# Optimization experiments

Measured on AMD Instinct MI355X. Metric: run time of the kernel, lower is better.

The kernel has to match this reference:

```python
import jax, jax.numpy as jnp
import numpy as np

B, N, H, NH = 2, 2048, 1024, 16
D = H // NH  # head_dim = 64


def setup_inputs() -> dict:
    key = jax.random.key(0)
    ks = jax.random.split(key, 12)
    s = 0.02
    inp = {
        'q': jax.random.normal(ks[0], (B, N, H), jnp.float32),
        'k': jax.random.normal(ks[1], (B, N, H), jnp.float32),
        'v': jax.random.normal(ks[2], (B, N, H), jnp.float32),
        # causal mask: 1 where attending allowed, 0 above diagonal
        'mask': jnp.tril(jnp.ones((N, N), jnp.float32))[None, None],
        'Wq': jax.random.normal(ks[3], (H, H), jnp.float32) * s,
        'bq': jnp.zeros((H,), jnp.float32),
        'Wk': jax.random.normal(ks[4], (H, H), jnp.float32) * s,
        'bk': jnp.zeros((H,), jnp.float32),
        'Wv': jax.random.normal(ks[5], (H, H), jnp.float32) * s,
        'bv': jnp.zeros((H,), jnp.float32),
        'Wp': jax.random.normal(ks[6], (H, H), jnp.float32) * s,
        'bp': jnp.zeros((H,), jnp.float32),
    }
    return inp


def _split_heads(x):
    # [b, n, (h d)] -> [b, h, n, d]
    b, n, _ = x.shape
    return x.reshape(b, n, NH, D).transpose(0, 2, 1, 3)


def reference(q, k, v, mask, Wq, bq, Wk, bk, Wv, bv, Wp, bp):
    # torch nn.Linear: x @ W.T + b
    Q = _split_heads(q @ Wq.T + bq)                      # [b, h, n, d]
    K = _split_heads(k @ Wk.T + bk)
    V = _split_heads(v @ Wv.T + bv)
    scores = jnp.einsum('bhnd,bhmd->bhnm', Q, K) / jnp.sqrt(jnp.float32(D))
    scores = jnp.where(mask == 0, -jnp.inf, scores)      # masked_fill
    attn = jax.nn.softmax(scores, axis=-1)
    out = jnp.einsum('bhnm,bhmd->bhnd', attn, V)         # [b, h, n, d]
    out = out.transpose(0, 2, 1, 3).reshape(q.shape[0], q.shape[1], H)
    # dropout is identity in eval mode
    return out @ Wp.T + bp
```

## Files before the change

kernel.cpp:

```cpp
#include <hip/hip_runtime.h>

typedef unsigned short u16;
typedef __attribute__((ext_vector_type(8))) short bf16x8;
typedef __attribute__((ext_vector_type(4))) short bf16x4;
typedef __attribute__((ext_vector_type(4))) float f32x4;

#define NB 2
#define SEQ 2048
#define HID 1024
#define NHEAD 16
#define HD 64
#define MROWS (NB * SEQ)

__device__ __forceinline__ u16 f2bf(float f) {
  union { float f; unsigned u; } x; x.f = f;
  unsigned r = x.u + 0x7fffu + ((x.u >> 16) & 1u);
  return (u16)(r >> 16);
}
__device__ __forceinline__ u16 f2bf_trunc(float f) {
  union { float f; unsigned u; } x; x.f = f;
  return (u16)(x.u >> 16);
}

#define GLOAD_LDS16(g, l)                                                   \
  __builtin_amdgcn_global_load_lds(                                         \
      (const __attribute__((address_space(1))) void*)(g),                   \
      (__attribute__((address_space(3))) void*)(l), 16, 0, 0)

__global__ __launch_bounds__(256)
void conv_all(const float* __restrict__ q, const float* __restrict__ k,
              const float* __restrict__ v, const float* __restrict__ wq,
              const float* __restrict__ wk, const float* __restrict__ wv,
              const float* __restrict__ wp, u16* __restrict__ qb,
              u16* __restrict__ kb, u16* __restrict__ vb,
              u16* __restrict__ wcat, u16* __restrict__ wpb)
{
  const int i = blockIdx.x * 256 + threadIdx.x;
  const float* s; u16* d;
  if (i < 1572864) {
    const int seg = i / 524288;
    const int off = i - seg * 524288;
    s = (seg == 0 ? q : seg == 1 ? k : v) + (size_t)off * 8;
    d = (seg == 0 ? qb : seg == 1 ? kb : vb) + (size_t)off * 8;
  } else {
    const int j = i - 1572864;
    const int seg = j / 131072;
    const int off = j - seg * 131072;
    s = (seg == 0 ? wq : seg == 1 ? wk : seg == 2 ? wv : wp) + (size_t)off * 8;
    d = (seg < 3 ? wcat + (size_t)seg * 1048576 : wpb) + (size_t)off * 8;
  }
  f32x4 a = *(const f32x4*)s;
  f32x4 b = *(const f32x4*)(s + 4);
  bf16x8 o;
#pragma unroll
  for (int j = 0; j < 4; ++j) { o[j] = (short)f2bf(a[j]); o[4 + j] = (short)f2bf(b[j]); }
  *(bf16x8*)d = o;
}

__global__ __launch_bounds__(256)
void gemm_qkv(const u16* __restrict__ A0, const u16* __restrict__ A1,
              const u16* __restrict__ A2, const u16* __restrict__ Wcat,
              const float* __restrict__ b0, const float* __restrict__ b1,
              const float* __restrict__ b2,
              u16* __restrict__ Qh, u16* __restrict__ Kh, u16* __restrict__ Vt,
              float qscale)
{
  __shared__ u16 As[2 * 128 * 64];
  __shared__ u16 Bs[2 * 128 * 64];
  const int p = blockIdx.x;
  const int c = p & 7;
  const int i_ = p >> 3;
  const int G = c * 12 + (i_ % 12);
  const int j = i_ / 12;
  const int g = G >> 5;
  const int m0 = (G & 31) * 128;
  const int n0 = (g * 8 + j) * 128;
  const u16* A = (g == 0) ? A0 : (g == 1) ? A1 : A2;
  const float* bias = (g == 0) ? b0 : (g == 1) ? b1 : b2;
  const int t = threadIdx.x, lane = t & 63, w = t >> 6;
  const int grp = lane >> 4, lr = lane & 15;
  const int wr = (w >> 1) * 64, wc = (w & 1) * 64;
  const int sw8 = lr & 7;

  f32x4 acc[4][4];
#pragma unroll
  for (int i = 0; i < 4; ++i)
#pragma unroll
    for (int j2 = 0; j2 < 4; ++j2) acc[i][j2] = (f32x4){0.f, 0.f, 0.f, 0.f};

  const int srow8 = lane >> 3;
  const int achunk = ((lane & 7) ^ srow8) * 8;
  const u16* ag = A + (size_t)(m0 + w * 32 + srow8) * HID + achunk;
  const u16* wg = Wcat + (size_t)(n0 + w * 32 + srow8) * HID + achunk;

#define STAGE(BI, K0)                                                \
  {                                                                  \
    const u16* ab = ag + (K0);                                       \
    const u16* wb = wg + (K0);                                       \
    u16* al = As + (BI) * 8192 + (w * 32) * 64;                      \
    u16* bl = Bs + (BI) * 8192 + (w * 32) * 64;                      \
    GLOAD_LDS16(ab, al);                                             \
    GLOAD_LDS16(ab + (size_t)8 * HID, al + 8 * 64);                  \
    GLOAD_LDS16(ab + (size_t)16 * HID, al + 16 * 64);                \
    GLOAD_LDS16(ab + (size_t)24 * HID, al + 24 * 64);                \
    GLOAD_LDS16(wb, bl);                                             \
    GLOAD_LDS16(wb + (size_t)8 * HID, bl + 8 * 64);                  \
    GLOAD_LDS16(wb + (size_t)16 * HID, bl + 16 * 64);                \
    GLOAD_LDS16(wb + (size_t)24 * HID, bl + 24 * 64);                \
  }

  STAGE(0, 0);

  for (int it = 0; it < 16; ++it) {
    const int cur = it & 1;
    asm volatile("s_waitcnt vmcnt(0)" ::: "memory");
    __builtin_amdgcn_s_barrier();
    __builtin_amdgcn_sched_barrier(0);
    asm volatile("" ::: "memory");
    if (it < 15) STAGE(cur ^ 1, (it + 1) * 64);
    const u16* Ab = As + cur * 8192;
    const u16* Bb = Bs + cur * 8192;
#pragma unroll
    for (int kh = 0; kh < 2; ++kh) {
      bf16x8 af[4], bf[4];
#pragma unroll
      for (int mi = 0; mi < 4; ++mi)
        af[mi] = *(const bf16x8*)&Ab[(wr + mi * 16 + lr) * 64 +
                                     (((kh * 4 + grp) ^ sw8) * 8)];
#pragma unroll
      for (int ni = 0; ni < 4; ++ni)
        bf[ni] = *(const bf16x8*)&Bb[(wc + ni * 16 + lr) * 64 +
                                     (((kh * 4 + grp) ^ sw8) * 8)];
      __builtin_amdgcn_s_setprio(1);
#pragma unroll
      for (int mi = 0; mi < 4; ++mi)
#pragma unroll
        for (int ni = 0; ni < 4; ++ni)
          acc[mi][ni] = __builtin_amdgcn_mfma_f32_16x16x32_bf16(
              af[mi], bf[ni], acc[mi][ni], 0, 0, 0);
      __builtin_amdgcn_s_setprio(0);
    }
  }
#undef STAGE

  const float scale = (g == 0) ? qscale : 1.f;
#pragma unroll
  for (int mi = 0; mi < 4; ++mi) {
#pragma unroll
    for (int ni = 0; ni < 4; ++ni) {
      const int nl = (n0 & (HID - 1)) + wc + ni * 16 + lr;
      const float bval = bias[nl];
      const int mb = m0 + wr + mi * 16 + grp * 4;
      const int h = nl >> 6, d = nl & (HD - 1);
      if (g == 2) {
        const int b = mb >> 11, nn = mb & (SEQ - 1);
        bf16x4 pk;
#pragma unroll
        for (int r = 0; r < 4; ++r)
          pk[r] = (short)f2bf(acc[mi][ni][r] + bval);
        *(bf16x4*)&Vt[((size_t)(b * NHEAD + h) * HD + d) * SEQ + nn] = pk;
      } else {
        u16* O = (g == 0) ? Qh : Kh;
#pragma unroll
        for (int r = 0; r < 4; ++r) {
          const int m = mb + r;
          const int b = m >> 11, nn = m & (SEQ - 1);
          O[((size_t)(b * NHEAD + h) * SEQ + nn) * HD + d] =
              f2bf((acc[mi][ni][r] + bval) * scale);
        }
      }
    }
  }
}

__global__ __launch_bounds__(256)
void gemm_proj(const u16* __restrict__ A, const u16* __restrict__ W,
               const float* __restrict__ bias, float* __restrict__ Op)
{
  __shared__ u16 As[2 * 128 * 64];
  __shared__ u16 Bs[2 * 128 * 64];
  const int p = blockIdx.x;
  const int c = p & 7;
  const int i_ = p >> 3;
  const int G = c * 4 + (i_ & 3);
  const int j = i_ >> 2;
  const int m0 = G * 128, n0 = j * 128;
  const int t = threadIdx.x, lane = t & 63, w = t >> 6;
  const int grp = lane >> 4, lr = lane & 15;
  const int wr = (w >> 1) * 64, wc = (w & 1) * 64;
  const int sw8 = lr & 7;

  f32x4 acc[4][4];
#pragma unroll
  for (int i = 0; i < 4; ++i)
#pragma unroll
    for (int j2 = 0; j2 < 4; ++j2) acc[i][j2] = (f32x4){0.f, 0.f, 0.f, 0.f};

  const int srow8 = lane >> 3;
  const int achunk = ((lane & 7) ^ srow8) * 8;
  const u16* ag = A + (size_t)(m0 + w * 32 + srow8) * HID + achunk;
  const u16* wg = W + (size_t)(n0 + w * 32 + srow8) * HID + achunk;

#define STAGE(BI, K0)                                                \
  {                                                                  \
    const u16* ab = ag + (K0);                                       \
    const u16* wb = wg + (K0);                                       \
    u16* al = As + (BI) * 8192 + (w * 32) * 64;                      \
    u16* bl = Bs + (BI) * 8192 + (w * 32) * 64;                      \
    GLOAD_LDS16(ab, al);                                             \
    GLOAD_LDS16(ab + (size_t)8 * HID, al + 8 * 64);                  \
    GLOAD_LDS16(ab + (size_t)16 * HID, al + 16 * 64);                \
    GLOAD_LDS16(ab + (size_t)24 * HID, al + 24 * 64);                \
    GLOAD_LDS16(wb, bl);                                             \
    GLOAD_LDS16(wb + (size_t)8 * HID, bl + 8 * 64);                  \
    GLOAD_LDS16(wb + (size_t)16 * HID, bl + 16 * 64);                \
    GLOAD_LDS16(wb + (size_t)24 * HID, bl + 24 * 64);                \
  }

  STAGE(0, 0);

  for (int it = 0; it < 16; ++it) {
    const int cur = it & 1;
    asm volatile("s_waitcnt vmcnt(0)" ::: "memory");
    __builtin_amdgcn_s_barrier();
    __builtin_amdgcn_sched_barrier(0);
    asm volatile("" ::: "memory");
    if (it < 15) STAGE(cur ^ 1, (it + 1) * 64);
    const u16* Ab = As + cur * 8192;
    const u16* Bb = Bs + cur * 8192;
#pragma unroll
    for (int kh = 0; kh < 2; ++kh) {
      bf16x8 af[4], bf[4];
#pragma unroll
      for (int mi = 0; mi < 4; ++mi)
        af[mi] = *(const bf16x8*)&Ab[(wr + mi * 16 + lr) * 64 +
                                     (((kh * 4 + grp) ^ sw8) * 8)];
#pragma unroll
      for (int ni = 0; ni < 4; ++ni)
        bf[ni] = *(const bf16x8*)&Bb[(wc + ni * 16 + lr) * 64 +
                                     (((kh * 4 + grp) ^ sw8) * 8)];
      __builtin_amdgcn_s_setprio(1);
#pragma unroll
      for (int mi = 0; mi < 4; ++mi)
#pragma unroll
        for (int ni = 0; ni < 4; ++ni)
          acc[mi][ni] = __builtin_amdgcn_mfma_f32_16x16x32_bf16(
              af[mi], bf[ni], acc[mi][ni], 0, 0, 0);
      __builtin_amdgcn_s_setprio(0);
    }
  }
#undef STAGE

#pragma unroll
  for (int mi = 0; mi < 4; ++mi) {
#pragma unroll
    for (int ni = 0; ni < 4; ++ni) {
      const int n = n0 + wc + ni * 16 + lr;
      const float bval = bias[n];
      const int mb = m0 + wr + mi * 16 + grp * 4;
#pragma unroll
      for (int r = 0; r < 4; ++r)
        Op[(size_t)(mb + r) * HID + n] = acc[mi][ni][r] + bval;
    }
  }
}

__global__ __launch_bounds__(512)
void attn_fwd(const u16* __restrict__ Q, const u16* __restrict__ K,
              const u16* __restrict__ Vt, u16* __restrict__ O)
{
  __shared__ u16 KB[2][4096];
  __shared__ u16 VB[2][4096];
  const int bh = blockIdx.y;
  const int t = threadIdx.x;
  const int w = t >> 6, lane = t & 63;
  const int grp = lane >> 4, lr = lane & 15;
  const int qtA = blockIdx.x;
  const int qtB = 15 - qtA;
  const int q0A = qtA * 128 + w * 16;
  const int q0B = qtB * 128 + w * 16;
  const int ntB = 2 * qtB + 2;
  const size_t base = (size_t)bh * SEQ * HD;
  const float NEGINF = -__builtin_inff();

  const int srow = lane >> 3;
  const int scol = (lane & 7) ^ srow;
  const u16* kg = K + base + (size_t)(w * 8 + srow) * HD + scol * 8;
  const u16* vg = Vt + base + (size_t)(w * 8 + srow) * SEQ + scol * 8;

  const bf16x8 aqA0 = *(const bf16x8*)&Q[base + (size_t)(q0A + lr) * HD + grp * 8];
  const bf16x8 aqA1 = *(const bf16x8*)&Q[base + (size_t)(q0A + lr) * HD + grp * 8 + 32];
  const bf16x8 aqB0 = *(const bf16x8*)&Q[base + (size_t)(q0B + lr) * HD + grp * 8];
  const bf16x8 aqB1 = *(const bf16x8*)&Q[base + (size_t)(q0B + lr) * HD + grp * 8 + 32];

  float lA = 0.f, lB = 0.f;
  f32x4 oA[4], oB[4];
#pragma unroll
  for (int c = 0; c < 4; ++c) {
    oA[c] = (f32x4){0.f, 0.f, 0.f, 0.f};
    oB[c] = (f32x4){0.f, 0.f, 0.f, 0.f};
  }

  const int idqA = q0A >> 6;
  const int idqB = q0B >> 6;
  const int sw = lr & 7;

#define STAGE(bi, j0)                                              \
  {                                                                \
    GLOAD_LDS16(kg + (size_t)(j0) * HD, &KB[bi][w * 512]);         \
    GLOAD_LDS16(vg + (j0), &VB[bi][w * 512]);                      \
  }

#define COMPUTE(Q0, AQ0, AQ1, OACC, LI, IDQ)                                  \
  do {                                                                        \
    f32x4 sv[4];                                                              \
    __builtin_amdgcn_s_setprio(1);                                            \
    _Pragma("unroll")                                                         \
    for (int st = 0; st < 4; ++st) {                                          \
      const int ro = (st * 16 + lr) * 64;                                     \
      bf16x8 k0 = *(const bf16x8*)&KB[bi][ro + ((grp ^ sw) * 8)];             \
      bf16x8 k1 = *(const bf16x8*)&KB[bi][ro + (((grp + 4) ^ sw) * 8)];       \
      f32x4 s = (f32x4){0.f, 0.f, 0.f, 0.f};                                  \
      s = __builtin_amdgcn_mfma_f32_16x16x32_bf16(k0, (AQ0), s, 0, 0, 0);     \
      s = __builtin_amdgcn_mfma_f32_16x16x32_bf16(k1, (AQ1), s, 0, 0, 0);     \
      sv[st] = s;                                                             \
    }                                                                         \
    __builtin_amdgcn_s_setprio(0);                                            \
    bf16x4 bv[4][4];                                                          \
    _Pragma("unroll")                                                         \
    for (int st = 0; st < 4; ++st)                                            \
      _Pragma("unroll")                                                       \
      for (int c = 0; c < 4; ++c)                                             \
        bv[st][c] = *(const bf16x4*)&VB[bi][(c * 16 + lr) * 64 +              \
                        (((st * 2 + (grp >> 1)) ^ sw) * 8) + (grp & 1) * 4];  \
    if (it == (IDQ)) {                                                        \
      const int j0 = it << 6, qg = (Q0) + lr;                                 \
      _Pragma("unroll")                                                       \
      for (int st = 0; st < 4; ++st)                                          \
        _Pragma("unroll")                                                     \
        for (int r = 0; r < 4; ++r)                                           \
          if (j0 + st * 16 + grp * 4 + r > qg) sv[st][r] = NEGINF;            \
    }                                                                         \
    float rs = 0.f;                                                           \
    _Pragma("unroll")                                                         \
    for (int st = 0; st < 4; ++st)                                            \
      _Pragma("unroll")                                                       \
      for (int r = 0; r < 4; ++r) {                                           \
        sv[st][r] = exp2f(sv[st][r]);                                         \
        rs += sv[st][r];                                                      \
      }                                                                       \
    (LI) += rs;                                                               \
    bf16x4 pa[4];                                                             \
    _Pragma("unroll")                                                         \
    for (int st = 0; st < 4; ++st)                                            \
      _Pragma("unroll")                                                       \
      for (int r = 0; r < 4; ++r) pa[st][r] = (short)f2bf_trunc(sv[st][r]);   \
    __builtin_amdgcn_s_setprio(1);                                            \
    _Pragma("unroll")                                                         \
    for (int st = 0; st < 4; ++st)                                            \
      _Pragma("unroll")                                                       \
      for (int c = 0; c < 4; ++c)                                             \
        (OACC)[c] = __builtin_amdgcn_mfma_f32_16x16x16bf16_1k(                \
            pa[st], bv[st][c], (OACC)[c], 0, 0, 0);                           \
    __builtin_amdgcn_s_setprio(0);                                            \
  } while (0)

  STAGE(0, 0);

  for (int it = 0; it < ntB; ++it) {
    const int bi = it & 1;
    asm volatile("s_waitcnt vmcnt(0)" ::: "memory");
    __builtin_amdgcn_s_barrier();
    __builtin_amdgcn_sched_barrier(0);
    asm volatile("" ::: "memory");
    if (it + 1 < ntB) STAGE(bi ^ 1, (it + 1) << 6);

    if (it <= idqB) COMPUTE(q0B, aqB0, aqB1, oB, lB, idqB);
    if (it <= idqA) COMPUTE(q0A, aqA0, aqA1, oA, lA, idqA);
  }
#undef STAGE
#undef COMPUTE

  lB += __shfl_xor(lB, 16);  lB += __shfl_xor(lB, 32);
  lA += __shfl_xor(lA, 16);  lA += __shfl_xor(lA, 32);

  const int b = bh >> 4, h = bh & (NHEAD - 1);
#pragma unroll
  for (int r = 0; r < 4; ++r) {
    const float liB = __shfl(lB, (lane & 48) + grp * 4 + r);
    const float invB = 1.f / liB;
    const int nB = q0B + grp * 4 + r;
#pragma unroll
    for (int c = 0; c < 4; ++c)
      O[(size_t)(b * SEQ + nB) * HID + h * HD + c * 16 + lr] =
          f2bf(oB[c][r] * invB);
    const float liA = __shfl(lA, (lane & 48) + grp * 4 + r);
    const float invA = 1.f / liA;
    const int nA = q0A + grp * 4 + r;
#pragma unroll
    for (int c = 0; c < 4; ++c)
      O[(size_t)(b * SEQ + nA) * HID + h * HD + c * 16 + lr] =
          f2bf(oA[c][r] * invA);
  }
}

extern "C" void kernel_launch(void* const* d_in, const int* in_sizes, int n_in,
                              void* d_out, int out_size, void* d_ws, size_t ws_size,
                              hipStream_t stream) {
  const float* q  = (const float*)d_in[0];
  const float* k  = (const float*)d_in[1];
  const float* v  = (const float*)d_in[2];
  const float* Wq = (const float*)d_in[4];
  const float* bq = (const float*)d_in[5];
  const float* Wk = (const float*)d_in[6];
  const float* bk = (const float*)d_in[7];
  const float* Wv = (const float*)d_in[8];
  const float* bv = (const float*)d_in[9];
  const float* Wp = (const float*)d_in[10];
  const float* bp = (const float*)d_in[11];
  float* out = (float*)d_out;

  char* ws = (char*)d_ws;
  u16* qb   = (u16*)(ws);
  u16* kb   = (u16*)(ws + ( 8u << 20));
  u16* vb   = (u16*)(ws + (16u << 20));
  u16* Wcat = (u16*)(ws + (24u << 20));
  u16* Wpb  = (u16*)(ws + (30u << 20));
  u16* Qh   = (u16*)(ws + (32u << 20));
  u16* Kh   = (u16*)(ws + (40u << 20));
  u16* Vt   = (u16*)(ws + (48u << 20));
  u16* AO   = qb;

  const float qscale = 0.125f * 1.4426950408889634f;

  conv_all<<<8192, 256, 0, stream>>>(q, k, v, Wq, Wk, Wv, Wp,
                                     qb, kb, vb, Wcat, Wpb);
  gemm_qkv<<<768, 256, 0, stream>>>(
      qb, kb, vb, Wcat, bq, bk, bv, Qh, Kh, Vt, qscale);
  attn_fwd<<<dim3(8, NB * NHEAD), 512, 0, stream>>>(Qh, Kh, Vt, AO);
  gemm_proj<<<256, 256, 0, stream>>>(AO, Wpb, bp, out);
}
```

Before: 131.8 us.

## Split attention key tiles across two blocks and add a combine kernel

Attention blocks now split the key/value tiles by parity, doubling the grid from 8 to 16 blocks per head. Each block writes unnormalized bf16 partial outputs and row sums to workspace. A new combine kernel adds the two partials, normalizes them and writes the head-merged attention output. The aim is better CU occupancy and load balance for the causal attention. The cost is an extra launch, extra global traffic for the partials, and an extra bf16 rounding step.

```diff
diff --git a/kernel.cpp b/kernel.cpp
--- a/kernel.cpp
+++ b/kernel.cpp
@@ -12,6 +12,9 @@
 #define HD 64
 #define MROWS (NB * SEQ)
 
+__device__ __forceinline__ float bf2f(u16 u) {
+  union { unsigned u; float f; } x; x.u = ((unsigned)u) << 16; return x.f;
+}
 __device__ __forceinline__ u16 f2bf(float f) {
   union { float f; unsigned u; } x; x.f = f;
   unsigned r = x.u + 0x7fffu + ((x.u >> 16) & 1u);
@@ -267,7 +270,8 @@
 
 __global__ __launch_bounds__(512)
 void attn_fwd(const u16* __restrict__ Q, const u16* __restrict__ K,
-              const u16* __restrict__ Vt, u16* __restrict__ O)
+              const u16* __restrict__ Vt, u16* __restrict__ parO,
+              float* __restrict__ parL)
 {
   __shared__ u16 KB[2][4096];
   __shared__ u16 VB[2][4096];
@@ -275,7 +279,9 @@
   const int t = threadIdx.x;
   const int w = t >> 6, lane = t & 63;
   const int grp = lane >> 4, lr = lane & 15;
-  const int qtA = blockIdx.x;
+  const int px = blockIdx.x;
+  const int parity = px & 1;
+  const int qtA = px >> 1;
   const int qtB = 15 - qtA;
   const int q0A = qtA * 128 + w * 16;
   const int q0B = qtB * 128 + w * 16;
@@ -365,15 +371,15 @@
     __builtin_amdgcn_s_setprio(0);                                            \
   } while (0)
 
-  STAGE(0, 0);
-
-  for (int it = 0; it < ntB; ++it) {
-    const int bi = it & 1;
+  STAGE(0, parity << 6);
+
+  for (int it = parity; it < ntB; it += 2) {
+    const int bi = ((it - parity) >> 1) & 1;
     asm volatile("s_waitcnt vmcnt(0)" ::: "memory");
     __builtin_amdgcn_s_barrier();
     __builtin_amdgcn_sched_barrier(0);
     asm volatile("" ::: "memory");
-    if (it + 1 < ntB) STAGE(bi ^ 1, (it + 1) << 6);
+    if (it + 2 < ntB) STAGE(bi ^ 1, (it + 2) << 6);
 
     if (it <= idqB) COMPUTE(q0B, aqB0, aqB1, oB, lB, idqB);
     if (it <= idqA) COMPUTE(q0A, aqA0, aqA1, oA, lA, idqA);
@@ -384,24 +390,44 @@
   lB += __shfl_xor(lB, 16);  lB += __shfl_xor(lB, 32);
   lA += __shfl_xor(lA, 16);  lA += __shfl_xor(lA, 32);
 
-  const int b = bh >> 4, h = bh & (NHEAD - 1);
+  const size_t pbase = (size_t)(parity * 32 + bh) * SEQ;
+  if (grp == 0) {
+    parL[pbase + q0B + lr] = lB;
+    parL[pbase + q0A + lr] = lA;
+  }
 #pragma unroll
   for (int r = 0; r < 4; ++r) {
-    const float liB = __shfl(lB, (lane & 48) + grp * 4 + r);
-    const float invB = 1.f / liB;
     const int nB = q0B + grp * 4 + r;
-#pragma unroll
-    for (int c = 0; c < 4; ++c)
-      O[(size_t)(b * SEQ + nB) * HID + h * HD + c * 16 + lr] =
-          f2bf(oB[c][r] * invB);
-    const float liA = __shfl(lA, (lane & 48) + grp * 4 + r);
-    const float invA = 1.f / liA;
     const int nA = q0A + grp * 4 + r;
 #pragma unroll
-    for (int c = 0; c < 4; ++c)
-      O[(size_t)(b * SEQ + nA) * HID + h * HD + c * 16 + lr] =
-          f2bf(oA[c][r] * invA);
-  }
+    for (int c = 0; c < 4; ++c) {
+      parO[(pbase + nB) * HD + c * 16 + lr] = f2bf(oB[c][r]);
+      parO[(pbase + nA) * HD + c * 16 + lr] = f2bf(oA[c][r]);
+    }
+  }
+}
+
+__global__ __launch_bounds__(256)
+void combine(const u16* __restrict__ parO, const float* __restrict__ parL,
+             u16* __restrict__ AO)
+{
+  const int i = blockIdx.x * 256 + threadIdx.x;
+  const int bh = i >> 14;
+  const int rem = i & 16383;
+  const int n = rem >> 3;
+  const int d0 = (rem & 7) * 8;
+  const size_t q0 = (size_t)bh * SEQ + n;
+  const float inv = 1.f / (parL[q0] + parL[q0 + 65536]);
+  const u16* p0 = parO + q0 * HD + d0;
+  const u16* p1 = p0 + (size_t)4194304;
+  bf16x8 a = *(const bf16x8*)p0;
+  bf16x8 b = *(const bf16x8*)p1;
+  bf16x8 o;
+#pragma unroll
+  for (int j = 0; j < 8; ++j)
+    o[j] = (short)f2bf((bf2f((u16)a[j]) + bf2f((u16)b[j])) * inv);
+  const int bb = bh >> 4, h = bh & 15;
+  *(bf16x8*)&AO[((size_t)(bb * SEQ + n)) * HID + h * HD + d0] = o;
 }
 
 extern "C" void kernel_launch(void* const* d_in, const int* in_sizes, int n_in,
@@ -421,15 +447,17 @@
   float* out = (float*)d_out;
 
   char* ws = (char*)d_ws;
-  u16* qb   = (u16*)(ws);
-  u16* kb   = (u16*)(ws + ( 8u << 20));
-  u16* vb   = (u16*)(ws + (16u << 20));
-  u16* Wcat = (u16*)(ws + (24u << 20));
-  u16* Wpb  = (u16*)(ws + (30u << 20));
-  u16* Qh   = (u16*)(ws + (32u << 20));
-  u16* Kh   = (u16*)(ws + (40u << 20));
-  u16* Vt   = (u16*)(ws + (48u << 20));
-  u16* AO   = qb;
+  u16*   qb   = (u16*)(ws);
+  u16*   kb   = (u16*)(ws + ( 8u << 20));
+  u16*   vb   = (u16*)(ws + (16u << 20));
+  u16*   Wcat = (u16*)(ws + (24u << 20));
+  u16*   Wpb  = (u16*)(ws + (30u << 20));
+  u16*   Qh   = (u16*)(ws + (32u << 20));
+  u16*   Kh   = (u16*)(ws + (40u << 20));
+  u16*   Vt   = (u16*)(ws + (48u << 20));
+  u16*   parO = (u16*)(ws);
+  float* parL = (float*)(ws + (17u << 20));
+  u16*   AO   = (u16*)(ws + (18u << 20));
 
   const float qscale = 0.125f * 1.4426950408889634f;
 
@@ -437,6 +465,7 @@
                                      qb, kb, vb, Wcat, Wpb);
   gemm_qkv<<<768, 256, 0, stream>>>(
       qb, kb, vb, Wcat, bq, bk, bv, Qh, Kh, Vt, qscale);
-  attn_fwd<<<dim3(8, NB * NHEAD), 512, 0, stream>>>(Qh, Kh, Vt, AO);
+  attn_fwd<<<dim3(16, NB * NHEAD), 512, 0, stream>>>(Qh, Kh, Vt, parO, parL);
+  combine<<<2048, 256, 0, stream>>>(parO, parL, AO);
   gemm_proj<<<256, 256, 0, stream>>>(AO, Wpb, bp, out);
 }
```

After: 123.6 us. 6.2% less time.
